# Optimization experiments

Measured on AMD Instinct MI355X. Metric: run time of the kernel, lower is better.

## Reference

```python
import jax, jax.numpy as jnp
import numpy as np

N_NODES = 100000
N_EDGES = 1600000
IN_CH = 128
HID_CH = 128
OUT_CH = 128
EDGE_DIM = 16
EPS = 1e-12


def _xavier(key, shape):
    fan_in, fan_out = shape[1], shape[0]
    a = jnp.sqrt(6.0 / (fan_in + fan_out))
    # torch Linear weight is [out, in]; we store transposed [in, out] for x @ W
    return jax.random.uniform(key, (shape[1], shape[0]), minval=-a, maxval=a, dtype=jnp.float32)


def setup_inputs() -> dict:
    key = jax.random.key(0)
    ks = jax.random.split(key, 8)
    x = jax.random.normal(ks[0], (N_NODES, IN_CH), dtype=jnp.float32)
    edge_index = jax.random.randint(ks[1], (2, N_EDGES), 0, N_NODES, dtype=jnp.int64)
    edge_attr = jax.random.normal(ks[2], (N_EDGES, EDGE_DIM), dtype=jnp.float32)
    # layer 1: message Linear(in+edge_dim -> hid), update Linear(in+hid -> hid)
    w_msg1 = _xavier(ks[3], (HID_CH, IN_CH + EDGE_DIM))
    b_msg1 = jnp.zeros((HID_CH,), jnp.float32)
    w_upd1 = _xavier(ks[4], (HID_CH, IN_CH + HID_CH))
    b_upd1 = jnp.zeros((HID_CH,), jnp.float32)
    bias1 = jnp.zeros((HID_CH,), jnp.float32)
    # layer 2: message Linear(hid+edge_dim -> out), update Linear(hid+out -> out)
    w_msg2 = _xavier(ks[5], (OUT_CH, HID_CH + EDGE_DIM))
    b_msg2 = jnp.zeros((OUT_CH,), jnp.float32)
    w_upd2 = _xavier(ks[6], (OUT_CH, HID_CH + OUT_CH))
    b_upd2 = jnp.zeros((OUT_CH,), jnp.float32)
    bias2 = jnp.zeros((OUT_CH,), jnp.float32)
    return {
        "x": x, "edge_index": edge_index, "edge_attr": edge_attr,
        "w_msg1": w_msg1, "b_msg1": b_msg1, "w_upd1": w_upd1, "b_upd1": b_upd1, "bias1": bias1,
        "w_msg2": w_msg2, "b_msg2": b_msg2, "w_upd2": w_upd2, "b_upd2": b_upd2, "bias2": bias2,
    }


def _layer(x, src, dst, edge_attr, w_msg, b_msg, w_upd, b_upd, bias):
    n = x.shape[0]
    # message: gather source node feats, concat edge feats, Linear + ReLU
    msg_in = jnp.concatenate([x[src], edge_attr], axis=1)        # [E, in+edge_dim]
    msg = jax.nn.relu(msg_in @ w_msg + b_msg)                     # [E, out]
    # scatter-mean aggregate at destination nodes
    summed = jax.ops.segment_sum(msg, dst, num_segments=n)        # [N, out]
    cnt = jax.ops.segment_sum(jnp.ones((msg.shape[0], 1), msg.dtype), dst, num_segments=n)
    agg = summed / jnp.maximum(cnt, 1.0)
    # update: concat self feats + aggregated, Linear
    out = jnp.concatenate([x, agg], axis=1) @ w_upd + b_upd       # [N, out]
    # F.normalize(p=2, dim=-1)
    norm = jnp.linalg.norm(out, axis=-1, keepdims=True)
    out = out / jnp.maximum(norm, EPS)
    return out + bias


def reference(x, edge_index, edge_attr,
              w_msg1, b_msg1, w_upd1, b_upd1, bias1,
              w_msg2, b_msg2, w_upd2, b_upd2, bias2):
    src, dst = edge_index[0], edge_index[1]
    h = _layer(x, src, dst, edge_attr, w_msg1, b_msg1, w_upd1, b_upd1, bias1)
    h = jax.nn.relu(h)  # inter-layer ReLU (dropout p=0.0 is identity)
    h = _layer(h, src, dst, edge_attr, w_msg2, b_msg2, w_upd2, b_upd2, bias2)
    return h
```

## Files before the change

### kernel.cpp

```cpp
#include <hip/hip_runtime.h>
#include <stdint.h>

#define N_NODES 100000
#define N_EDGES 1600000
#define CH 128
#define EDGE_DIM 16
#define KUPD 256
#define NPW 8

typedef __attribute__((ext_vector_type(8))) short short8v;
typedef __attribute__((ext_vector_type(4))) float f32x4;

__device__ __forceinline__ float bf2f(ushort u) {
  union { uint i; float f; } c; c.i = ((uint)u) << 16; return c.f;
}
__device__ __forceinline__ ushort f2bf(float f) {
  union { float f; uint i; } c; c.f = f;
  return (ushort)((c.i + 0x7FFFu + ((c.i >> 16) & 1u)) >> 16);
}
__device__ __forceinline__ float ldf(const void* p, int f32, size_t i) {
  return f32 ? ((const float*)p)[i] : bf2f(((const ushort*)p)[i]);
}
__device__ __forceinline__ float2 ld2(const void* p, int f32, size_t pi) {
  if (f32) return ((const float2*)p)[pi];
  uint u = ((const uint*)p)[pi];
  return make_float2(bf2f((ushort)(u & 0xFFFF)), bf2f((ushort)(u >> 16)));
}
__device__ __forceinline__ float4 ld4(const void* p, int f32, size_t qi) {
  if (f32) return ((const float4*)p)[qi];
  uint2 u = ((const uint2*)p)[qi];
  float4 r;
  r.x = bf2f((ushort)(u.x & 0xFFFF)); r.y = bf2f((ushort)(u.x >> 16));
  r.z = bf2f((ushort)(u.y & 0xFFFF)); r.w = bf2f((ushort)(u.y >> 16));
  return r;
}
__device__ __forceinline__ int resolve_f32(int x_sel, const int* flags) {
  return (x_sel == 2) ? 1 : (x_sel == 1 ? flags[1] : 0);
}
__device__ __forceinline__ int kmap(int MAP, int g, int j, int step) {
  return MAP ? (step * 32 + 8 * g + j)
             : (step * 32 + 16 * (j >> 2) + 4 * g + (j & 3));
}

__global__ __launch_bounds__(256) void detect_probe(const int* __restrict__ ei,
                                                    const ushort* __restrict__ xu,
                                                    const ushort* __restrict__ eau,
                                                    const ushort* __restrict__ wu,
                                                    int* __restrict__ flags) {
  __shared__ ushort A[16 * 32];
  __shared__ ushort B[32 * 16];
  int any = 0, fx = 0, fe = 0, fw = 0;
  for (int i = threadIdx.x; i < 4096; i += 256) any |= ei[2 * i + 1];
  for (int i = threadIdx.x; i < 16384; i += 256) {
    fx |= (((xu[2 * i] >> 7) & 0xFF) == 0xFF);
    fe |= (((eau[2 * i] >> 7) & 0xFF) == 0xFF);
  }
  for (int i = threadIdx.x; i < 8192; i += 256) {
    fw |= (((wu[2 * i] >> 7) & 0xFF) == 0xFF);
  }
  if (any) atomicOr(flags + 0, 1);
  if (fx)  atomicOr(flags + 1, 1);
  if (fe)  atomicOr(flags + 2, 1);
  if (fw)  atomicOr(flags + 3, 1);
  for (int idx = threadIdx.x; idx < 512; idx += 256) {
    int i = idx >> 5, k = idx & 31;
    A[idx] = f2bf((float)((i * 5 + k * 3) % 13 - 6));
    int k2 = idx >> 4, c = idx & 15;
    B[idx] = f2bf((float)((k2 * 7 + c * 11) % 15 - 7));
  }
  __syncthreads();
  if (threadIdx.x < 64) {
    const int lane = threadIdx.x;
    const int col = lane & 15, g = lane >> 4;
    float cr[4];
#pragma unroll
    for (int r = 0; r < 4; ++r) {
      int row = g * 4 + r;
      float s = 0.f;
      for (int k = 0; k < 32; ++k) s += bf2f(A[row * 32 + k]) * bf2f(B[k * 16 + col]);
      cr[r] = s;
    }
    int win = 2;
    for (int MAP = 0; MAP < 2; ++MAP) {
      if (win != 2) break;
      short8v a, b;
#pragma unroll
      for (int j = 0; j < 8; ++j) {
        int k = kmap(MAP, g, j, 0);
        a[j] = (short)A[(lane & 15) * 32 + k];
        b[j] = (short)B[k * 16 + col];
      }
      f32x4 z = {0.f, 0.f, 0.f, 0.f};
      f32x4 d = __builtin_amdgcn_mfma_f32_16x16x32_bf16(a, b, z, 0, 0, 0);
      int good = 1;
#pragma unroll
      for (int r = 0; r < 4; ++r) good &= (d[r] == cr[r]);
      if (__all(good)) win = MAP;
    }
    if (lane == 0) flags[4] = win;
  }
}

__device__ __forceinline__ void load_edge(const int* __restrict__ ei, int i32, int e,
                                          int& s, int& d) {
  if (i32) { s = ei[e]; d = ei[N_EDGES + e]; }
  else     { s = ei[2 * e]; d = ei[2 * N_EDGES + 2 * e]; }
  s = min(max(s, 0), N_NODES - 1);
  d = min(max(d, 0), N_NODES - 1);
}

__global__ __launch_bounds__(256) void count_kernel(const int* __restrict__ ei,
                                                    const int* __restrict__ flags,
                                                    int* __restrict__ cnt) {
  int e = blockIdx.x * 256 + threadIdx.x;
  if (e >= N_EDGES) return;
  int d = flags[0] ? ei[N_EDGES + e] : ei[2 * N_EDGES + 2 * e];
  d = min(max(d, 0), N_NODES - 1);
  atomicAdd(&cnt[d], 1);
}

__global__ __launch_bounds__(1024) void scan_kernel(const int* __restrict__ cnt,
                                                    int* __restrict__ rowptr) {
  __shared__ int part[1024];
  const int t = threadIdx.x;
  const int CHUNK = (N_NODES + 1023) / 1024;
  int base = t * CHUNK;
  int lim = min(base + CHUNK, N_NODES);
  int s = 0;
  for (int i = base; i < lim; ++i) s += cnt[i];
  part[t] = s;
  __syncthreads();
  for (int off = 1; off < 1024; off <<= 1) {
    int v = (t >= off) ? part[t - off] : 0;
    __syncthreads();
    part[t] += v;
    __syncthreads();
  }
  int excl = (t == 0) ? 0 : part[t - 1];
  for (int i = base; i < lim; ++i) { rowptr[i] = excl; excl += cnt[i]; }
  if (t == 1023) rowptr[N_NODES] = part[1023];
}

__global__ __launch_bounds__(256) void scatter_kernel(const int* __restrict__ ei,
                                                      const int* __restrict__ flags,
                                                      const int* __restrict__ rowptr,
                                                      int* __restrict__ fill,
                                                      int2* __restrict__ sev) {
  int e = blockIdx.x * 256 + threadIdx.x;
  if (e >= N_EDGES) return;
  int s, d;
  load_edge(ei, flags[0], e, s, d);
  int pos = atomicAdd(&fill[d], 1);
  sev[rowptr[d] + pos] = make_int2(s, e);
}

__global__ __launch_bounds__(256) void wshuf_all(const void* __restrict__ wu1,
                                                 const void* __restrict__ wu2,
                                                 const void* __restrict__ wm1,
                                                 const void* __restrict__ wm2,
                                                 const int* __restrict__ flags,
                                                 ushort* __restrict__ ou1,
                                                 ushort* __restrict__ ou2,
                                                 ushort* __restrict__ om1,
                                                 ushort* __restrict__ om2,
                                                 ushort* __restrict__ oz1,
                                                 ushort* __restrict__ oz2,
                                                 uint* __restrict__ ybf) {
  const int MAP = flags[4], wf = flags[3];
  if (MAP == 2) return;
  int tid = blockIdx.x * 256 + threadIdx.x;
  if (tid >= 13376) return;
  int gg = tid >> 6, lane = tid & 63;
  int col16 = lane & 15, g = lane >> 4;
  if (gg == 208) {
    ybf[(size_t)N_NODES * 64 + lane] = 0u;
    return;
  }
  if (gg >= 192) {
    int l = gg - 192;
    const void* W = (l < 8) ? wm1 : wm2;
    ushort* dst = (l < 8) ? oz1 : oz2;
    int t = l & 7;
#pragma unroll
    for (int j = 0; j < 8; ++j) {
      int k = kmap(MAP, g, j, 0);
      ushort v = (k < 16) ? f2bf(ldf(W, wf, (size_t)(CH + k) * CH + t * 16 + col16)) : (ushort)0;
      dst[(size_t)t * 512 + lane * 8 + j] = v;
    }
    return;
  }
  const void* W; ushort* dst; int t, step, ts;
  if (gg < 64)       { W = wu1; dst = ou1; int l = gg;       t = l >> 3; step = l & 7; ts = t * 8 + step; }
  else if (gg < 128) { W = wu2; dst = ou2; int l = gg - 64;  t = l >> 3; step = l & 7; ts = t * 8 + step; }
  else if (gg < 160) { W = wm1; dst = om1; int l = gg - 128; t = l >> 2; step = l & 3; ts = t * 4 + step; }
  else               { W = wm2; dst = om2; int l = gg - 160; t = l >> 2; step = l & 3; ts = t * 4 + step; }
  int col = t * 16 + col16;
#pragma unroll
  for (int j = 0; j < 8; ++j) {
    int k = kmap(MAP, g, j, step);
    dst[(size_t)ts * 512 + lane * 8 + j] = f2bf(ldf(W, wf, (size_t)k * CH + col));
  }
}

template <int MAP>
__device__ __forceinline__ void gemm_mfma_body(const void* __restrict__ x, int xf,
                                               const ushort* __restrict__ wshm,
                                               const void* __restrict__ bmsg, int wf,
                                               uint* __restrict__ ybf,
                                               int n0, int lane, char* lds) {
  const int srow = lane >> 2;
  const int q = lane & 3;
  {
    uint sw = (uint)((srow & 7) << 4);
#pragma unroll
    for (int i = 0; i < 8; ++i) {
      int qi = q + 4 * i;
      float4 v = ld4(x, xf, (size_t)(n0 + srow) * 32 + qi);
      uint2 pk;
      pk.x = (uint)f2bf(v.x) | ((uint)f2bf(v.y) << 16);
      pk.y = (uint)f2bf(v.z) | ((uint)f2bf(v.w) << 16);
      *(uint2*)(lds + (((uint)srow * 256u + (uint)qi * 8u) ^ sw)) = pk;
    }
  }
  asm volatile("s_waitcnt lgkmcnt(0)" ::: "memory");
  __builtin_amdgcn_sched_barrier(0);

  const int col = lane & 15, g = lane >> 4;
  const int ra = lane & 15;
  const uint asw = (uint)((ra & 7) << 4);
  f32x4 acc[8];
#pragma unroll
  for (int t = 0; t < 8; ++t) acc[t] = (f32x4){0.f, 0.f, 0.f, 0.f};

#pragma unroll
  for (int step = 0; step < 4; ++step) {
    short8v a;
    if (MAP) {
      uint byte = (uint)ra * 256u + (uint)(step * 32 + 8 * g) * 2u;
      *(uint4*)&a = *(const uint4*)(lds + (byte ^ asw));
    } else {
      uint b0 = (uint)ra * 256u + (uint)(step * 32 + 4 * g) * 2u;
      uint b1 = b0 + 32u;
      uint2 lo = *(const uint2*)(lds + (b0 ^ asw));
      uint2 hi = *(const uint2*)(lds + (b1 ^ asw));
      uint4 pk = make_uint4(lo.x, lo.y, hi.x, hi.y);
      *(uint4*)&a = pk;
    }
#pragma unroll
    for (int t = 0; t < 8; ++t) {
      short8v b = *(const short8v*)(wshm + ((size_t)(t * 4 + step) * 512 + lane * 8));
      acc[t] = __builtin_amdgcn_mfma_f32_16x16x32_bf16(a, b, acc[t], 0, 0, 0);
    }
  }

#pragma unroll
  for (int u = 0; u < 4; ++u) {
    float b0v = ldf(bmsg, wf, u * 32 + col);
    float b1v = ldf(bmsg, wf, u * 32 + 16 + col);
#pragma unroll
    for (int r = 0; r < 4; ++r) {
      uint pk = (uint)f2bf(acc[2 * u][r] + b0v) | ((uint)f2bf(acc[2 * u + 1][r] + b1v) << 16);
      ybf[(uint)(n0 + g * 4 + r) * 64u + (uint)(u * 16 + col)] = pk;
    }
  }
}

__device__ __forceinline__ void gemm_f32_body(const void* __restrict__ x, int xf,
                                              const void* __restrict__ W, int wf,
                                              const void* __restrict__ b,
                                              uint* __restrict__ ybf,
                                              int wave_n0, int lane, char* ldsc) {
  float* xs = (float*)ldsc;
  for (int c = 0; c < 2; ++c) {
    int n0 = wave_n0 + c * 8;
#pragma unroll
    for (int r = 0; r < NPW; ++r) {
      float2 a = ld2(x, xf, (size_t)(n0 + r) * 64 + lane);
      xs[r * 128 + 2 * lane]     = a.x;
      xs[r * 128 + 2 * lane + 1] = a.y;
    }
    asm volatile("s_waitcnt lgkmcnt(0)" ::: "memory");
    __builtin_amdgcn_sched_barrier(0);
    float acc0[NPW], acc1[NPW];
#pragma unroll
    for (int r = 0; r < NPW; ++r) { acc0[r] = 0.f; acc1[r] = 0.f; }
#pragma unroll 4
    for (int k = 0; k < CH; k += 2) {
      float2 w0 = ld2(W, wf, (size_t)k * 64 + lane);
      float2 w1 = ld2(W, wf, (size_t)(k + 1) * 64 + lane);
#pragma unroll
      for (int r = 0; r < NPW; ++r) {
        float2 a = *(const float2*)&xs[r * 128 + k];
        acc0[r] += a.x * w0.x;
        acc1[r] += a.x * w0.y;
        acc0[r] += a.y * w1.x;
        acc1[r] += a.y * w1.y;
      }
    }
    float2 bb = ld2(b, wf, lane);
#pragma unroll
    for (int r = 0; r < NPW; ++r) {
      uint pk = (uint)f2bf(acc0[r] + bb.x) | ((uint)f2bf(acc1[r] + bb.y) << 16);
      ybf[(uint)(n0 + r) * 64u + (uint)lane] = pk;
    }
  }
}

__global__ __launch_bounds__(256) void gemm_node(const void* __restrict__ x, int x_sel,
                                                 const ushort* __restrict__ wshm,
                                                 const void* __restrict__ W,
                                                 const void* __restrict__ b,
                                                 const int* __restrict__ flags,
                                                 uint* __restrict__ ybf) {
  __shared__ char lds[16384];
  const int wave = threadIdx.x >> 6;
  const int lane = threadIdx.x & 63;
  const int wid = blockIdx.x * 4 + wave;
  if (wid >= N_NODES / 16) return;
  const int n0 = wid * 16;
  const int xf = resolve_f32(x_sel, flags), wf = flags[3];
  const int MAP = flags[4];
  char* myl = lds + wave * 4096;
  if (MAP == 0)      gemm_mfma_body<0>(x, xf, wshm, b, wf, ybf, n0, lane, myl);
  else if (MAP == 1) gemm_mfma_body<1>(x, xf, wshm, b, wf, ybf, n0, lane, myl);
  else               gemm_f32_body(x, xf, W, wf, b, ybf, n0, lane, myl);
}

template <int MAP>
__device__ __forceinline__ void agg_mfma_body(const uint* __restrict__ ybf,
                                              const void* __restrict__ ea, int ef,
                                              const ushort* __restrict__ wze,
                                              const int* __restrict__ rowptr,
                                              const int2* __restrict__ sev,
                                              float* __restrict__ agg,
                                              int n0, int lane) {
  const int col = lane & 15, g = lane >> 4;
  short8v bfr[8];
#pragma unroll
  for (int t = 0; t < 8; ++t)
    bfr[t] = *(const short8v*)(wze + ((size_t)t * 512 + lane * 8));

  for (int ni = 0; ni < 8; ++ni) {
    const int n = n0 + ni;
    const int beg = rowptr[n], end = rowptr[n + 1];
    f32x4 acc[8];
#pragma unroll
    for (int t = 0; t < 8; ++t) acc[t] = (f32x4){0.f, 0.f, 0.f, 0.f};

    for (int j0 = beg; j0 < end; j0 += 16) {
      int jr = j0 + col;
      uint amask = (jr < end) ? 0xFFFFFFFFu : 0u;
      if (jr > end - 1) jr = end - 1;
      int2 p = sev[jr];
      int e = p.y;
      short8v a;
      if (MAP == 1) {
        if (g < 2) {
          float4 qa = ld4(ea, ef, (size_t)e * 4 + 2 * g);
          float4 qb = ld4(ea, ef, (size_t)e * 4 + 2 * g + 1);
          uint4 pk;
          pk.x = ((uint)f2bf(qa.x) | ((uint)f2bf(qa.y) << 16)) & amask;
          pk.y = ((uint)f2bf(qa.z) | ((uint)f2bf(qa.w) << 16)) & amask;
          pk.z = ((uint)f2bf(qb.x) | ((uint)f2bf(qb.y) << 16)) & amask;
          pk.w = ((uint)f2bf(qb.z) | ((uint)f2bf(qb.w) << 16)) & amask;
          *(uint4*)&a = pk;
        } else {
          *(uint4*)&a = make_uint4(0, 0, 0, 0);
        }
      } else {
        float4 q = ld4(ea, ef, (size_t)e * 4 + g);
        uint4 pk;
        pk.x = ((uint)f2bf(q.x) | ((uint)f2bf(q.y) << 16)) & amask;
        pk.y = ((uint)f2bf(q.z) | ((uint)f2bf(q.w) << 16)) & amask;
        pk.z = 0; pk.w = 0;
        *(uint4*)&a = pk;
      }
      f32x4 zz = {0.f, 0.f, 0.f, 0.f};
      f32x4 zf[8];
#pragma unroll
      for (int t = 0; t < 8; ++t)
        zf[t] = __builtin_amdgcn_mfma_f32_16x16x32_bf16(a, bfr[t], zz, 0, 0, 0);

      int myS = p.x;
#pragma unroll
      for (int r = 0; r < 4; ++r) {
        int slot = g * 4 + r;
        int s = __shfl(myS, slot);
        if (j0 + slot >= end) s = N_NODES;
        uint yb = (uint)s * 64u + (uint)col;
#pragma unroll
        for (int u = 0; u < 4; ++u) {
          uint yu = ybf[yb + (uint)u * 16u];
          float lo = bf2f((ushort)(yu & 0xFFFF));
          float hi = bf2f((ushort)(yu >> 16));
          acc[2 * u][r]     += fmaxf(lo + zf[2 * u][r], 0.f);
          acc[2 * u + 1][r] += fmaxf(hi + zf[2 * u + 1][r], 0.f);
        }
      }
    }
    float part[8];
#pragma unroll
    for (int t = 0; t < 8; ++t) {
      part[t] = (acc[t][0] + acc[t][1]) + (acc[t][2] + acc[t][3]);
      part[t] += __shfl_xor(part[t], 16);
      part[t] += __shfl_xor(part[t], 32);
    }
    agg[(size_t)n * CH + (size_t)(2 * g) * 16 + col]     = part[2 * g];
    agg[(size_t)n * CH + (size_t)(2 * g + 1) * 16 + col] = part[2 * g + 1];
  }
}

__device__ __forceinline__ void agg_f32_body(const uint* __restrict__ ybf,
                                             const void* __restrict__ ea, int ef,
                                             const void* __restrict__ W, int wf,
                                             const int* __restrict__ rowptr,
                                             const int2* __restrict__ sev,
                                             float* __restrict__ agg,
                                             int n0, int lane) {
  const int c0 = 2 * lane, c1 = c0 + 1;
  float wex[EDGE_DIM], wey[EDGE_DIM];
#pragma unroll
  for (int k = 0; k < EDGE_DIM; ++k) {
    wex[k] = ldf(W, wf, (size_t)(CH + k) * CH + c0);
    wey[k] = ldf(W, wf, (size_t)(CH + k) * CH + c1);
  }
  for (int ni = 0; ni < 8; ++ni) {
    const int n = n0 + ni;
    const int beg = rowptr[n], end = rowptr[n + 1];
    float acc0 = 0.f, acc1 = 0.f;
    for (int j = beg; j < end; ++j) {
      int2 p = sev[j];
      int s = __builtin_amdgcn_readfirstlane(p.x), e = __builtin_amdgcn_readfirstlane(p.y);
      uint yu = ybf[(size_t)s * 64 + lane];
      float4 q0 = ld4(ea, ef, (size_t)e * 4 + 0);
      float4 q1 = ld4(ea, ef, (size_t)e * 4 + 1);
      float4 q2 = ld4(ea, ef, (size_t)e * 4 + 2);
      float4 q3 = ld4(ea, ef, (size_t)e * 4 + 3);
      float av[16] = {q0.x, q0.y, q0.z, q0.w, q1.x, q1.y, q1.z, q1.w,
                      q2.x, q2.y, q2.z, q2.w, q3.x, q3.y, q3.z, q3.w};
      float z0 = 0.f, z1 = 0.f;
#pragma unroll
      for (int k = 0; k < EDGE_DIM; ++k) {
        z0 += av[k] * wex[k];
        z1 += av[k] * wey[k];
      }
      acc0 += fmaxf(bf2f((ushort)(yu & 0xFFFF)) + z0, 0.f);
      acc1 += fmaxf(bf2f((ushort)(yu >> 16)) + z1, 0.f);
    }
    agg[(size_t)n * CH + c0] = acc0;
    agg[(size_t)n * CH + c1] = acc1;
  }
}

__global__ __launch_bounds__(256) void agg_csr(const uint* __restrict__ ybf,
                                               const void* __restrict__ ea,
                                               const ushort* __restrict__ wze,
                                               const void* __restrict__ W,
                                               const int* __restrict__ rowptr,
                                               const int2* __restrict__ sev,
                                               const int* __restrict__ flags,
                                               float* __restrict__ agg) {
  const int wave = threadIdx.x >> 6;
  const int lane = threadIdx.x & 63;
  const int n0 = (blockIdx.x * 4 + wave) * 8;
  const int ef = flags[2], wf = flags[3], MAP = flags[4];
  if (MAP == 0)      agg_mfma_body<0>(ybf, ea, ef, wze, rowptr, sev, agg, n0, lane);
  else if (MAP == 1) agg_mfma_body<1>(ybf, ea, ef, wze, rowptr, sev, agg, n0, lane);
  else               agg_f32_body(ybf, ea, ef, W, wf, rowptr, sev, agg, n0, lane);
}

template <int MAP>
__device__ __forceinline__ void upd_mfma_body(const void* __restrict__ x, int xf,
                                              const float* __restrict__ agg,
                                              const int* __restrict__ rowptr,
                                              const ushort* __restrict__ wsh,
                                              const void* __restrict__ bupd, int wf,
                                              const void* __restrict__ bias,
                                              float* __restrict__ out, int relu,
                                              int n0, int lane, char* lds) {
  const int srow = lane >> 2;
  const int q = lane & 3;
  {
    int c = rowptr[n0 + srow + 1] - rowptr[n0 + srow];
    float inv = 1.f / (float)(c > 1 ? c : 1);
    uint sw = (uint)((srow & 7) << 4);
#pragma unroll
    for (int i = 0; i < 8; ++i) {
      int qi = q + 4 * i;
      float4 v = ld4(x, xf, (size_t)(n0 + srow) * 32 + qi);
      uint2 pk;
      pk.x = (uint)f2bf(v.x) | ((uint)f2bf(v.y) << 16);
      pk.y = (uint)f2bf(v.z) | ((uint)f2bf(v.w) << 16);
      *(uint2*)(lds + (((uint)srow * 512u + (uint)qi * 8u) ^ sw)) = pk;
      float4 w = ((const float4*)agg)[(size_t)(n0 + srow) * 32 + qi];
      uint2 pk2;
      pk2.x = (uint)f2bf(w.x * inv) | ((uint)f2bf(w.y * inv) << 16);
      pk2.y = (uint)f2bf(w.z * inv) | ((uint)f2bf(w.w * inv) << 16);
      *(uint2*)(lds + (((uint)srow * 512u + 256u + (uint)qi * 8u) ^ sw)) = pk2;
    }
  }
  asm volatile("s_waitcnt lgkmcnt(0)" ::: "memory");
  __builtin_amdgcn_sched_barrier(0);

  const int col = lane & 15, g = lane >> 4;
  const int ra = lane & 15;
  const uint asw = (uint)((ra & 7) << 4);
  f32x4 acc[8];
#pragma unroll
  for (int t = 0; t < 8; ++t) acc[t] = (f32x4){0.f, 0.f, 0.f, 0.f};

#pragma unroll
  for (int step = 0; step < 8; ++step) {
    short8v a;
    if (MAP) {
      uint byte = (uint)ra * 512u + (uint)(step * 32 + 8 * g) * 2u;
      *(uint4*)&a = *(const uint4*)(lds + (byte ^ asw));
    } else {
      uint b0 = (uint)ra * 512u + (uint)(step * 32 + 4 * g) * 2u;
      uint b1 = b0 + 32u;
      uint2 lo = *(const uint2*)(lds + (b0 ^ asw));
      uint2 hi = *(const uint2*)(lds + (b1 ^ asw));
      uint4 pk = make_uint4(lo.x, lo.y, hi.x, hi.y);
      *(uint4*)&a = pk;
    }
#pragma unroll
    for (int t = 0; t < 8; ++t) {
      short8v b = *(const short8v*)(wsh + ((size_t)(t * 8 + step) * 512 + lane * 8));
      acc[t] = __builtin_amdgcn_mfma_f32_16x16x32_bf16(a, b, acc[t], 0, 0, 0);
    }
  }

  float bu[8], bi[8];
#pragma unroll
  for (int t = 0; t < 8; ++t) {
    bu[t] = ldf(bupd, wf, t * 16 + col);
    bi[t] = ldf(bias, wf, t * 16 + col);
  }
  float raw[8][4];
  float ss[4] = {0.f, 0.f, 0.f, 0.f};
#pragma unroll
  for (int t = 0; t < 8; ++t)
#pragma unroll
    for (int r = 0; r < 4; ++r) {
      float v = acc[t][r] + bu[t];
      raw[t][r] = v;
      ss[r] += v * v;
    }
#pragma unroll
  for (int r = 0; r < 4; ++r)
#pragma unroll
    for (int o = 1; o < 16; o <<= 1) ss[r] += __shfl_xor(ss[r], o);
#pragma unroll
  for (int r = 0; r < 4; ++r) {
    float inv = 1.0f / fmaxf(sqrtf(ss[r]), 1e-12f);
    int row = g * 4 + r;
#pragma unroll
    for (int t = 0; t < 8; ++t) {
      float o = raw[t][r] * inv + bi[t];
      if (relu) o = fmaxf(o, 0.f);
      out[(size_t)(n0 + row) * CH + t * 16 + col] = o;
    }
  }
}

__device__ __forceinline__ void upd_f32_body(const void* __restrict__ x, int xf,
                                             const float* __restrict__ agg,
                                             const int* __restrict__ rowptr,
                                             const void* __restrict__ W, int wf,
                                             const void* __restrict__ bupd,
                                             const void* __restrict__ bias,
                                             float* __restrict__ out, int relu,
                                             int wave_n0, int lane, char* ldsc) {
  float* xs = (float*)ldsc;
  for (int c = 0; c < 2; ++c) {
    int n0 = wave_n0 + c * 8;
#pragma unroll
    for (int r = 0; r < NPW; ++r) {
      int n = n0 + r;
      float2 a = ld2(x, xf, (size_t)n * 64 + lane);
      xs[r * 256 + 2 * lane]     = a.x;
      xs[r * 256 + 2 * lane + 1] = a.y;
      int cd = rowptr[n + 1] - rowptr[n];
      float inv = 1.f / (float)(cd > 1 ? cd : 1);
      xs[r * 256 + CH + 2 * lane]     = agg[(size_t)n * CH + 2 * lane] * inv;
      xs[r * 256 + CH + 2 * lane + 1] = agg[(size_t)n * CH + 2 * lane + 1] * inv;
    }
    asm volatile("s_waitcnt lgkmcnt(0)" ::: "memory");
    __builtin_amdgcn_sched_barrier(0);

    float acc0[NPW], acc1[NPW];
#pragma unroll
    for (int r = 0; r < NPW; ++r) { acc0[r] = 0.f; acc1[r] = 0.f; }
#pragma unroll 4
    for (int k = 0; k < KUPD; k += 2) {
      float2 w0 = ld2(W, wf, (size_t)k * 64 + lane);
      float2 w1 = ld2(W, wf, (size_t)(k + 1) * 64 + lane);
#pragma unroll
      for (int r = 0; r < NPW; ++r) {
        float2 a = *(const float2*)&xs[r * 256 + k];
        acc0[r] += a.x * w0.x;
        acc1[r] += a.x * w0.y;
        acc0[r] += a.y * w1.x;
        acc1[r] += a.y * w1.y;
      }
    }
    float2 b  = ld2(bupd, wf, lane);
    float2 bi = ld2(bias, wf, lane);
#pragma unroll
    for (int r = 0; r < NPW; ++r) {
      float r0 = acc0[r] + b.x;
      float r1 = acc1[r] + b.y;
      float sq = r0 * r0 + r1 * r1;
#pragma unroll
      for (int o = 32; o; o >>= 1) sq += __shfl_xor(sq, o);
      float innv = 1.0f / fmaxf(sqrtf(sq), 1e-12f);
      float o0 = r0 * innv + bi.x;
      float o1 = r1 * innv + bi.y;
      if (relu) { o0 = fmaxf(o0, 0.f); o1 = fmaxf(o1, 0.f); }
      size_t n = (size_t)(n0 + r);
      out[n * CH + 2 * lane]     = o0;
      out[n * CH + 2 * lane + 1] = o1;
    }
  }
}

__global__ __launch_bounds__(256) void upd_fused(const void* __restrict__ x, int x_sel,
                                                 const float* __restrict__ agg,
                                                 const int* __restrict__ rowptr,
                                                 const ushort* __restrict__ wsh,
                                                 const void* __restrict__ W,
                                                 const void* __restrict__ bupd,
                                                 const void* __restrict__ bias,
                                                 const int* __restrict__ flags,
                                                 float* __restrict__ out,
                                                 int relu) {
  __shared__ char lds[32768];
  const int wave = threadIdx.x >> 6;
  const int lane = threadIdx.x & 63;
  const int wid = blockIdx.x * 4 + wave;
  if (wid >= N_NODES / 16) return;
  const int n0 = wid * 16;
  const int xf = resolve_f32(x_sel, flags), wf = flags[3];
  const int MAP = flags[4];
  char* myl = lds + wave * 8192;
  if (MAP == 0)
    upd_mfma_body<0>(x, xf, agg, rowptr, wsh, bupd, wf, bias, out, relu, n0, lane, myl);
  else if (MAP == 1)
    upd_mfma_body<1>(x, xf, agg, rowptr, wsh, bupd, wf, bias, out, relu, n0, lane, myl);
  else
    upd_f32_body(x, xf, agg, rowptr, W, wf, bupd, bias, out, relu, n0, lane, myl);
}

extern "C" void kernel_launch(void* const* d_in, const int* in_sizes, int n_in,
                              void* d_out, int out_size, void* d_ws, size_t ws_size,
                              hipStream_t stream) {
  const void* x   = d_in[0];
  const int*  ei  = (const int*)d_in[1];
  const void* ea  = d_in[2];
  const void* wm1 = d_in[3];
  const void* bm1 = d_in[4];
  const void* wu1 = d_in[5];
  const void* bu1 = d_in[6];
  const void* bi1 = d_in[7];
  const void* wm2 = d_in[8];
  const void* bm2 = d_in[9];
  const void* wu2 = d_in[10];
  const void* bu2 = d_in[11];
  const void* bi2 = d_in[12];
  float* out = (float*)d_out;

  char* base = (char*)d_ws;
  size_t off = 0;
  auto alloc = [&](size_t b) { size_t o = off; off += (b + 255) & ~(size_t)255; return o; };
  size_t flags_o = alloc(32);
  size_t cnt_o   = alloc((size_t)N_NODES * 4);
  size_t fill_o  = alloc((size_t)N_NODES * 4);
  size_t zero_end = off;
  size_t rowp_o  = alloc((size_t)(N_NODES + 1) * 4);
  size_t sev_o   = alloc((size_t)N_EDGES * 8);
  size_t agg_o   = alloc((size_t)N_NODES * CH * 4);
  size_t y_o     = alloc((size_t)(N_NODES + 1) * CH * 2);
  size_t wsh1_o  = alloc((size_t)4096 * 8 * 2);
  size_t wsh2_o  = alloc((size_t)4096 * 8 * 2);
  size_t wshm1_o = alloc((size_t)2048 * 8 * 2);
  size_t wshm2_o = alloc((size_t)2048 * 8 * 2);
  size_t wze1_o  = alloc((size_t)512 * 8 * 2);
  size_t wze2_o  = alloc((size_t)512 * 8 * 2);
  (void)ws_size; (void)n_in; (void)in_sizes; (void)out_size;

  int*    flags = (int*)(base + flags_o);
  int*    cntp  = (int*)(base + cnt_o);
  int*    fillp = (int*)(base + fill_o);
  int*    rowp  = (int*)(base + rowp_o);
  int2*   sevp  = (int2*)(base + sev_o);
  float*  aggp  = (float*)(base + agg_o);
  uint*   ybfp  = (uint*)(base + y_o);
  ushort* wsh1  = (ushort*)(base + wsh1_o);
  ushort* wsh2  = (ushort*)(base + wsh2_o);
  ushort* wshm1 = (ushort*)(base + wshm1_o);
  ushort* wshm2 = (ushort*)(base + wshm2_o);
  ushort* wze1  = (ushort*)(base + wze1_o);
  ushort* wze2  = (ushort*)(base + wze2_o);
  float*  hp    = out;

  hipMemsetAsync(base, 0, zero_end, stream);
  detect_probe<<<1, 256, 0, stream>>>(ei, (const ushort*)x, (const ushort*)ea,
                                      (const ushort*)wm1, flags);
  count_kernel<<<(N_EDGES + 255) / 256, 256, 0, stream>>>(ei, flags, cntp);
  scan_kernel<<<1, 1024, 0, stream>>>(cntp, rowp);
  scatter_kernel<<<(N_EDGES + 255) / 256, 256, 0, stream>>>(ei, flags, rowp, fillp, sevp);
  wshuf_all<<<53, 256, 0, stream>>>(wu1, wu2, wm1, wm2, flags,
                                    wsh1, wsh2, wshm1, wshm2, wze1, wze2, ybfp);

  const int agrid = N_NODES / 32;
  const int wgrid = (N_NODES / 16 + 3) / 4;

  gemm_node<<<wgrid, 256, 0, stream>>>(x, 1, wshm1, wm1, bm1, flags, ybfp);
  agg_csr<<<agrid, 256, 0, stream>>>(ybfp, ea, wze1, wm1, rowp, sevp, flags, aggp);
  upd_fused<<<wgrid, 256, 0, stream>>>(x, 1, aggp, rowp, wsh1, wu1, bu1, bi1, flags, hp, 1);

  gemm_node<<<wgrid, 256, 0, stream>>>(hp, 2, wshm2, wm2, bm2, flags, ybfp);
  agg_csr<<<agrid, 256, 0, stream>>>(ybfp, ea, wze2, wm2, rowp, sevp, flags, aggp);
  upd_fused<<<wgrid, 256, 0, stream>>>(hp, 2, aggp, rowp, wsh2, wu2, bu2, bi2, flags, out, 0);
}
```

Before: 968.5 us.

## Store edge attrs, aggregates and hidden features as bf16 to cut traffic

The scatter kernel now converts edge_attr to packed bf16 once, and both aggregation passes read that copy instead of re-converting fp32 per edge. The aggregation kernel applies the mean division and writes bf16 aggregates, so the update kernel loads half-width data and no longer needs rowptr. Layer 1's update writes the hidden state as bf16, which layer 2's gemm and update consume directly. The aim is to reduce global memory traffic and conversion work. The cost is an extra edge-sized bf16 buffer plus the added write in the scatter kernel. The fp32 fallback paths keep separate pointers.

```diff
diff --git a/kernel.cpp b/kernel.cpp
--- a/kernel.cpp
+++ b/kernel.cpp
@@ -142,16 +142,25 @@
 }
 
 __global__ __launch_bounds__(256) void scatter_kernel(const int* __restrict__ ei,
+                                                      const void* __restrict__ ea,
                                                       const int* __restrict__ flags,
                                                       const int* __restrict__ rowptr,
                                                       int* __restrict__ fill,
-                                                      int2* __restrict__ sev) {
+                                                      int2* __restrict__ sev,
+                                                      uint* __restrict__ eabf) {
   int e = blockIdx.x * 256 + threadIdx.x;
   if (e >= N_EDGES) return;
   int s, d;
   load_edge(ei, flags[0], e, s, d);
   int pos = atomicAdd(&fill[d], 1);
   sev[rowptr[d] + pos] = make_int2(s, e);
+  const int ef = flags[2];
+#pragma unroll
+  for (int qv = 0; qv < 4; ++qv) {
+    float4 v = ld4(ea, ef, (size_t)e * 4 + qv);
+    eabf[(size_t)e * 8 + 2 * qv]     = (uint)f2bf(v.x) | ((uint)f2bf(v.y) << 16);
+    eabf[(size_t)e * 8 + 2 * qv + 1] = (uint)f2bf(v.z) | ((uint)f2bf(v.w) << 16);
+  }
 }
 
 __global__ __launch_bounds__(256) void wshuf_all(const void* __restrict__ wu1,
@@ -215,14 +224,18 @@
 #pragma unroll
     for (int i = 0; i < 8; ++i) {
       int qi = q + 4 * i;
-      float4 v = ld4(x, xf, (size_t)(n0 + srow) * 32 + qi);
       uint2 pk;
-      pk.x = (uint)f2bf(v.x) | ((uint)f2bf(v.y) << 16);
-      pk.y = (uint)f2bf(v.z) | ((uint)f2bf(v.w) << 16);
+      if (xf) {
+        float4 v = ((const float4*)x)[(size_t)(n0 + srow) * 32 + qi];
+        pk.x = (uint)f2bf(v.x) | ((uint)f2bf(v.y) << 16);
+        pk.y = (uint)f2bf(v.z) | ((uint)f2bf(v.w) << 16);
+      } else {
+        pk = ((const uint2*)x)[(size_t)(n0 + srow) * 32 + qi];
+      }
       *(uint2*)(lds + (((uint)srow * 256u + (uint)qi * 8u) ^ sw)) = pk;
     }
   }
-  asm volatile("s_waitcnt lgkmcnt(0)" ::: "memory");
+  asm volatile("s_waitcnt lgkmcnt(0) vmcnt(0)" ::: "memory");
   __builtin_amdgcn_sched_barrier(0);
 
   const int col = lane & 15, g = lane >> 4;
@@ -306,7 +319,8 @@
   }
 }
 
-__global__ __launch_bounds__(256) void gemm_node(const void* __restrict__ x, int x_sel,
+__global__ __launch_bounds__(256) void gemm_node(const void* __restrict__ xa, int sa,
+                                                 const void* __restrict__ xb, int sb,
                                                  const ushort* __restrict__ wshm,
                                                  const void* __restrict__ W,
                                                  const void* __restrict__ b,
@@ -318,21 +332,21 @@
   const int wid = blockIdx.x * 4 + wave;
   if (wid >= N_NODES / 16) return;
   const int n0 = wid * 16;
-  const int xf = resolve_f32(x_sel, flags), wf = flags[3];
+  const int wf = flags[3];
   const int MAP = flags[4];
   char* myl = lds + wave * 4096;
-  if (MAP == 0)      gemm_mfma_body<0>(x, xf, wshm, b, wf, ybf, n0, lane, myl);
-  else if (MAP == 1) gemm_mfma_body<1>(x, xf, wshm, b, wf, ybf, n0, lane, myl);
-  else               gemm_f32_body(x, xf, W, wf, b, ybf, n0, lane, myl);
+  if (MAP == 0)      gemm_mfma_body<0>(xa, resolve_f32(sa, flags), wshm, b, wf, ybf, n0, lane, myl);
+  else if (MAP == 1) gemm_mfma_body<1>(xa, resolve_f32(sa, flags), wshm, b, wf, ybf, n0, lane, myl);
+  else               gemm_f32_body(xb, resolve_f32(sb, flags), W, wf, b, ybf, n0, lane, myl);
 }
 
 template <int MAP>
 __device__ __forceinline__ void agg_mfma_body(const uint* __restrict__ ybf,
-                                              const void* __restrict__ ea, int ef,
+                                              const uint* __restrict__ eabf,
                                               const ushort* __restrict__ wze,
                                               const int* __restrict__ rowptr,
                                               const int2* __restrict__ sev,
-                                              float* __restrict__ agg,
+                                              ushort* __restrict__ aggbf,
                                               int n0, int lane) {
   const int col = lane & 15, g = lane >> 4;
   short8v bfr[8];
@@ -355,23 +369,19 @@
       int e = p.y;
       short8v a;
       if (MAP == 1) {
+        uint4 pk;
         if (g < 2) {
-          float4 qa = ld4(ea, ef, (size_t)e * 4 + 2 * g);
-          float4 qb = ld4(ea, ef, (size_t)e * 4 + 2 * g + 1);
-          uint4 pk;
-          pk.x = ((uint)f2bf(qa.x) | ((uint)f2bf(qa.y) << 16)) & amask;
-          pk.y = ((uint)f2bf(qa.z) | ((uint)f2bf(qa.w) << 16)) & amask;
-          pk.z = ((uint)f2bf(qb.x) | ((uint)f2bf(qb.y) << 16)) & amask;
-          pk.w = ((uint)f2bf(qb.z) | ((uint)f2bf(qb.w) << 16)) & amask;
-          *(uint4*)&a = pk;
+          pk = ((const uint4*)eabf)[(size_t)e * 2 + g];
+          pk.x &= amask; pk.y &= amask; pk.z &= amask; pk.w &= amask;
         } else {
-          *(uint4*)&a = make_uint4(0, 0, 0, 0);
+          pk = make_uint4(0, 0, 0, 0);
         }
+        *(uint4*)&a = pk;
       } else {
-        float4 q = ld4(ea, ef, (size_t)e * 4 + g);
+        uint2 qv = ((const uint2*)eabf)[(size_t)e * 4 + g];
         uint4 pk;
-        pk.x = ((uint)f2bf(q.x) | ((uint)f2bf(q.y) << 16)) & amask;
-        pk.y = ((uint)f2bf(q.z) | ((uint)f2bf(q.w) << 16)) & amask;
+        pk.x = qv.x & amask;
+        pk.y = qv.y & amask;
         pk.z = 0; pk.w = 0;
         *(uint4*)&a = pk;
       }
@@ -398,6 +408,8 @@
         }
       }
     }
+    int c = end - beg;
+    float inv = 1.f / (float)(c > 1 ? c : 1);
     float part[8];
 #pragma unroll
     for (int t = 0; t < 8; ++t) {
@@ -405,8 +417,8 @@
       part[t] += __shfl_xor(part[t], 16);
       part[t] += __shfl_xor(part[t], 32);
     }
-    agg[(size_t)n * CH + (size_t)(2 * g) * 16 + col]     = part[2 * g];
-    agg[(size_t)n * CH + (size_t)(2 * g + 1) * 16 + col] = part[2 * g + 1];
+    aggbf[(size_t)n * CH + 32 * g + col]      = f2bf(part[2 * g] * inv);
+    aggbf[(size_t)n * CH + 32 * g + 16 + col] = f2bf(part[2 * g + 1] * inv);
   }
 }
 
@@ -453,53 +465,54 @@
 }
 
 __global__ __launch_bounds__(256) void agg_csr(const uint* __restrict__ ybf,
+                                               const uint* __restrict__ eabf,
                                                const void* __restrict__ ea,
                                                const ushort* __restrict__ wze,
                                                const void* __restrict__ W,
                                                const int* __restrict__ rowptr,
                                                const int2* __restrict__ sev,
                                                const int* __restrict__ flags,
-                                               float* __restrict__ agg) {
+                                               ushort* __restrict__ aggbf,
+                                               float* __restrict__ aggf) {
   const int wave = threadIdx.x >> 6;
   const int lane = threadIdx.x & 63;
   const int n0 = (blockIdx.x * 4 + wave) * 8;
   const int ef = flags[2], wf = flags[3], MAP = flags[4];
-  if (MAP == 0)      agg_mfma_body<0>(ybf, ea, ef, wze, rowptr, sev, agg, n0, lane);
-  else if (MAP == 1) agg_mfma_body<1>(ybf, ea, ef, wze, rowptr, sev, agg, n0, lane);
-  else               agg_f32_body(ybf, ea, ef, W, wf, rowptr, sev, agg, n0, lane);
+  if (MAP == 0)      agg_mfma_body<0>(ybf, eabf, wze, rowptr, sev, aggbf, n0, lane);
+  else if (MAP == 1) agg_mfma_body<1>(ybf, eabf, wze, rowptr, sev, aggbf, n0, lane);
+  else               agg_f32_body(ybf, ea, ef, W, wf, rowptr, sev, aggf, n0, lane);
 }
 
 template <int MAP>
 __device__ __forceinline__ void upd_mfma_body(const void* __restrict__ x, int xf,
-                                              const float* __restrict__ agg,
-                                              const int* __restrict__ rowptr,
+                                              const ushort* __restrict__ aggbf,
                                               const ushort* __restrict__ wsh,
                                               const void* __restrict__ bupd, int wf,
                                               const void* __restrict__ bias,
-                                              float* __restrict__ out, int relu,
+                                              float* __restrict__ outf,
+                                              ushort* __restrict__ outbf, int relu,
                                               int n0, int lane, char* lds) {
   const int srow = lane >> 2;
   const int q = lane & 3;
   {
-    int c = rowptr[n0 + srow + 1] - rowptr[n0 + srow];
-    float inv = 1.f / (float)(c > 1 ? c : 1);
     uint sw = (uint)((srow & 7) << 4);
 #pragma unroll
     for (int i = 0; i < 8; ++i) {
       int qi = q + 4 * i;
-      float4 v = ld4(x, xf, (size_t)(n0 + srow) * 32 + qi);
       uint2 pk;
-      pk.x = (uint)f2bf(v.x) | ((uint)f2bf(v.y) << 16);
-      pk.y = (uint)f2bf(v.z) | ((uint)f2bf(v.w) << 16);
+      if (xf) {
+        float4 v = ((const float4*)x)[(size_t)(n0 + srow) * 32 + qi];
+        pk.x = (uint)f2bf(v.x) | ((uint)f2bf(v.y) << 16);
+        pk.y = (uint)f2bf(v.z) | ((uint)f2bf(v.w) << 16);
+      } else {
+        pk = ((const uint2*)x)[(size_t)(n0 + srow) * 32 + qi];
+      }
       *(uint2*)(lds + (((uint)srow * 512u + (uint)qi * 8u) ^ sw)) = pk;
-      float4 w = ((const float4*)agg)[(size_t)(n0 + srow) * 32 + qi];
-      uint2 pk2;
-      pk2.x = (uint)f2bf(w.x * inv) | ((uint)f2bf(w.y * inv) << 16);
-      pk2.y = (uint)f2bf(w.z * inv) | ((uint)f2bf(w.w * inv) << 16);
-      *(uint2*)(lds + (((uint)srow * 512u + 256u + (uint)qi * 8u) ^ sw)) = pk2;
-    }
-  }
-  asm volatile("s_waitcnt lgkmcnt(0)" ::: "memory");
+      uint2 pa = ((const uint2*)aggbf)[(size_t)(n0 + srow) * 32 + qi];
+      *(uint2*)(lds + (((uint)srow * 512u + 256u + (uint)qi * 8u) ^ sw)) = pa;
+    }
+  }
+  asm volatile("s_waitcnt lgkmcnt(0) vmcnt(0)" ::: "memory");
   __builtin_amdgcn_sched_barrier(0);
 
   const int col = lane & 15, g = lane >> 4;
@@ -558,7 +571,8 @@
     for (int t = 0; t < 8; ++t) {
       float o = raw[t][r] * inv + bi[t];
       if (relu) o = fmaxf(o, 0.f);
-      out[(size_t)(n0 + row) * CH + t * 16 + col] = o;
+      if (outbf) outbf[(size_t)(n0 + row) * CH + t * 16 + col] = f2bf(o);
+      else       outf[(size_t)(n0 + row) * CH + t * 16 + col] = o;
     }
   }
 }
@@ -624,15 +638,18 @@
   }
 }
 
-__global__ __launch_bounds__(256) void upd_fused(const void* __restrict__ x, int x_sel,
-                                                 const float* __restrict__ agg,
+__global__ __launch_bounds__(256) void upd_fused(const void* __restrict__ xa, int sa,
+                                                 const void* __restrict__ xb, int sb,
+                                                 const ushort* __restrict__ aggbf,
+                                                 const float* __restrict__ aggf,
                                                  const int* __restrict__ rowptr,
                                                  const ushort* __restrict__ wsh,
                                                  const void* __restrict__ W,
                                                  const void* __restrict__ bupd,
                                                  const void* __restrict__ bias,
                                                  const int* __restrict__ flags,
-                                                 float* __restrict__ out,
+                                                 float* __restrict__ outf,
+                                                 ushort* __restrict__ outbf,
                                                  int relu) {
   __shared__ char lds[32768];
   const int wave = threadIdx.x >> 6;
@@ -640,15 +657,15 @@
   const int wid = blockIdx.x * 4 + wave;
   if (wid >= N_NODES / 16) return;
   const int n0 = wid * 16;
-  const int xf = resolve_f32(x_sel, flags), wf = flags[3];
+  const int wf = flags[3];
   const int MAP = flags[4];
   char* myl = lds + wave * 8192;
   if (MAP == 0)
-    upd_mfma_body<0>(x, xf, agg, rowptr, wsh, bupd, wf, bias, out, relu, n0, lane, myl);
+    upd_mfma_body<0>(xa, resolve_f32(sa, flags), aggbf, wsh, bupd, wf, bias, outf, outbf, relu, n0, lane, myl);
   else if (MAP == 1)
-    upd_mfma_body<1>(x, xf, agg, rowptr, wsh, bupd, wf, bias, out, relu, n0, lane, myl);
+    upd_mfma_body<1>(xa, resolve_f32(sa, flags), aggbf, wsh, bupd, wf, bias, outf, outbf, relu, n0, lane, myl);
   else
-    upd_f32_body(x, xf, agg, rowptr, W, wf, bupd, bias, out, relu, n0, lane, myl);
+    upd_f32_body(xb, resolve_f32(sb, flags), aggf, rowptr, W, wf, bupd, bias, outf, relu, n0, lane, myl);
 }
 
 extern "C" void kernel_launch(void* const* d_in, const int* in_sizes, int n_in,
@@ -680,6 +697,8 @@
   size_t sev_o   = alloc((size_t)N_EDGES * 8);
   size_t agg_o   = alloc((size_t)N_NODES * CH * 4);
   size_t y_o     = alloc((size_t)(N_NODES + 1) * CH * 2);
+  size_t hbf_o   = alloc((size_t)N_NODES * CH * 2);
+  size_t eabf_o  = alloc((size_t)N_EDGES * EDGE_DIM * 2);
   size_t wsh1_o  = alloc((size_t)4096 * 8 * 2);
   size_t wsh2_o  = alloc((size_t)4096 * 8 * 2);
   size_t wshm1_o = alloc((size_t)2048 * 8 * 2);
@@ -693,8 +712,11 @@
   int*    fillp = (int*)(base + fill_o);
   int*    rowp  = (int*)(base + rowp_o);
   int2*   sevp  = (int2*)(base + sev_o);
-  float*  aggp  = (float*)(base + agg_o);
+  float*  aggf  = (float*)(base + agg_o);
+  ushort* aggbf = (ushort*)(base + agg_o);
   uint*   ybfp  = (uint*)(base + y_o);
+  ushort* hbfp  = (ushort*)(base + hbf_o);
+  uint*   eabfp = (uint*)(base + eabf_o);
   ushort* wsh1  = (ushort*)(base + wsh1_o);
   ushort* wsh2  = (ushort*)(base + wsh2_o);
   ushort* wshm1 = (ushort*)(base + wshm1_o);
@@ -708,18 +730,23 @@
                                       (const ushort*)wm1, flags);
   count_kernel<<<(N_EDGES + 255) / 256, 256, 0, stream>>>(ei, flags, cntp);
   scan_kernel<<<1, 1024, 0, stream>>>(cntp, rowp);
-  scatter_kernel<<<(N_EDGES + 255) / 256, 256, 0, stream>>>(ei, flags, rowp, fillp, sevp);
+  scatter_kernel<<<(N_EDGES + 255) / 256, 256, 0, stream>>>(ei, ea, flags, rowp,
+                                                            fillp, sevp, eabfp);
   wshuf_all<<<53, 256, 0, stream>>>(wu1, wu2, wm1, wm2, flags,
                                     wsh1, wsh2, wshm1, wshm2, wze1, wze2, ybfp);
 
   const int agrid = N_NODES / 32;
   const int wgrid = (N_NODES / 16 + 3) / 4;
 
-  gemm_node<<<wgrid, 256, 0, stream>>>(x, 1, wshm1, wm1, bm1, flags, ybfp);
-  agg_csr<<<agrid, 256, 0, stream>>>(ybfp, ea, wze1, wm1, rowp, sevp, flags, aggp);
-  upd_fused<<<wgrid, 256, 0, stream>>>(x, 1, aggp, rowp, wsh1, wu1, bu1, bi1, flags, hp, 1);
-
-  gemm_node<<<wgrid, 256, 0, stream>>>(hp, 2, wshm2, wm2, bm2, flags, ybfp);
-  agg_csr<<<agrid, 256, 0, stream>>>(ybfp, ea, wze2, wm2, rowp, sevp, flags, aggp);
-  upd_fused<<<wgrid, 256, 0, stream>>>(hp, 2, aggp, rowp, wsh2, wu2, bu2, bi2, flags, out, 0);
-}
+  gemm_node<<<wgrid, 256, 0, stream>>>(x, 1, x, 1, wshm1, wm1, bm1, flags, ybfp);
+  agg_csr<<<agrid, 256, 0, stream>>>(ybfp, eabfp, ea, wze1, wm1, rowp, sevp, flags,
+                                     aggbf, aggf);
+  upd_fused<<<wgrid, 256, 0, stream>>>(x, 1, x, 1, aggbf, aggf, rowp, wsh1, wu1,
+                                       bu1, bi1, flags, hp, hbfp, 1);
+
+  gemm_node<<<wgrid, 256, 0, stream>>>(hbfp, 0, hp, 2, wshm2, wm2, bm2, flags, ybfp);
+  agg_csr<<<agrid, 256, 0, stream>>>(ybfp, eabfp, ea, wze2, wm2, rowp, sevp, flags,
+                                     aggbf, aggf);
+  upd_fused<<<wgrid, 256, 0, stream>>>(hbfp, 0, hp, 2, aggbf, aggf, rowp, wsh2, wu2,
+                                       bu2, bi2, flags, out, (ushort*)nullptr, 0);
+}
```

Measured after the change: 1.076 ms. 11.1% more time.
